# Kernel tuning notes

Hardware: AMD Instinct MI355X
Metric: run time of the kernel (lower is better)

The kernel has to match this reference:

```python
import jax, jax.numpy as jnp
import numpy as np

K = 3  # inferred kernel size (28->26->pool->13->11->pool->5 matches 32*5*5 FC input)


def _patches(x, k=K):
    # x: (N,C,H,W) -> (N,C,k*k,OH,OW) valid patches, stride 1
    N, C, H, W = x.shape
    OH, OW = H - k + 1, W - k + 1
    return jnp.stack(
        [x[:, :, i:i + OH, j:j + OW] for i in range(k) for j in range(k)], axis=2
    )


def _maxpool2(x):
    N, C, H, W = x.shape
    H2, W2 = H // 2, W // 2
    x = x[:, :, :H2 * 2, :W2 * 2].reshape(N, C, H2, 2, W2, 2)
    return x.max(axis=(3, 5))


def _lc2d(x, w, b):
    # unshared-weight locally connected conv: w (O,C,k*k,OH,OW), b (O,OH,OW)
    p = _patches(x)  # (N,C,k*k,OH,OW)
    return jnp.einsum('nckij,ockij->noij', p, w) + b


def setup_inputs():
    key = jax.random.key(0)
    ks = jax.random.split(key, 9)
    s = 0.05
    return {
        'x': jax.random.normal(ks[0], (4096, 1, 28, 28), jnp.float32),
        'w1': jax.random.normal(ks[1], (16, 1, 9, 26, 26), jnp.float32) * s,
        'b1': jax.random.normal(ks[2], (16, 26, 26), jnp.float32) * s,
        'w2': jax.random.normal(ks[3], (32, 16, 9, 11, 11), jnp.float32) * s,
        'b2': jax.random.normal(ks[4], (32, 11, 11), jnp.float32) * s,
        'fc1_w': jax.random.normal(ks[5], (32 * 5 * 5, 128), jnp.float32) * s,
        'fc1_b': jax.random.normal(ks[6], (128,), jnp.float32) * s,
        'fc2_w': jax.random.normal(ks[7], (128, 10), jnp.float32) * s,
        'fc2_b': jax.random.normal(ks[8], (10,), jnp.float32) * s,
    }


def reference(x, w1, b1, w2, b2, fc1_w, fc1_b, fc2_w, fc2_b):
    h = _maxpool2(jax.nn.relu(_lc2d(x, w1, b1)))      # (N,16,13,13)
    h = _maxpool2(jax.nn.relu(_lc2d(h, w2, b2)))      # (N,32,5,5)
    h = h.reshape(h.shape[0], -1)                      # (N,800)
    h = jax.nn.relu(h @ fc1_w + fc1_b)                 # (N,128)
    return h @ fc2_w + fc2_b                           # (N,10)
```

## Files before the change

kernel.cpp:

```cpp
#include <hip/hip_runtime.h>

#define NB 4096

typedef __attribute__((ext_vector_type(8))) short s8v;
typedef __attribute__((ext_vector_type(4))) float f4v;

#define H1B_OFF 6422528u
#define H2B_OFF 28573696u
#define W2B_OFF 35127296u
#define B2R_OFF 36765696u
#define W1B_OFF 36778496u
#define B1R_OFF 37470720u
#define WFB_OFF 37513984u

__device__ __forceinline__ unsigned short f2bf(float f) {
  unsigned int u = __builtin_bit_cast(unsigned int, f);
  u += 0x7fffu + ((u >> 16) & 1u);
  return (unsigned short)(u >> 16);
}

__global__ __launch_bounds__(256) void k_prep(const float* __restrict__ w1,
                                              const float* __restrict__ b1,
                                              const float* __restrict__ w2,
                                              const float* __restrict__ b2,
                                              const float* __restrict__ f1w,
                                              short* __restrict__ w1b,
                                              float* __restrict__ b1r,
                                              short* __restrict__ w2b,
                                              float* __restrict__ b2r,
                                              short* __restrict__ wfb) {
  const int bx = blockIdx.x;
  if (bx < 169) {
    const int q = bx * 256 + threadIdx.x;
    const int l = q & 63;
    const int cv = (q >> 6) & 3;
    const int pos = q >> 8;
    const int o = l & 15;
    const int i = pos / 13, j = pos % 13;
    const int dy = cv >> 1, dx = cv & 1;
    unsigned short v[8];
    #pragma unroll
    for (int t = 0; t < 8; t++) {
      const int k = (l >> 4) * 8 + t;
      float f = 0.f;
      if (k < 16) {
        const int py = k >> 2, px = k & 3;
        const int ky = py - dy, kx = px - dx;
        if (ky >= 0 && ky < 3 && kx >= 0 && kx < 3)
          f = w1[(o * 9 + ky * 3 + kx) * 676 + (2 * i + dy) * 26 + 2 * j + dx];
      }
      v[t] = f2bf(f);
    }
    *reinterpret_cast<s8v*>(&w1b[q * 8]) = *reinterpret_cast<const s8v*>(v);
  } else if (bx < 212) {
    const int idx = (bx - 169) * 256 + threadIdx.x;
    if (idx < 10816) {
      const int cv = idx & 3;
      const int o = (idx >> 2) & 15;
      const int pos = idx >> 6;
      const int i = pos / 13, j = pos % 13;
      b1r[idx] = b1[(o * 26 + 2 * i + (cv >> 1)) * 26 + 2 * j + (cv & 1)];
    }
  } else if (bx < 612) {
    const int q = (bx - 212) * 256 + threadIdx.x;
    const int l = q & 63;
    const int ot = (q >> 6) & 1;
    const int s = (q >> 7) & 7;
    const int cv = (q >> 10) & 3;
    const int pos = q >> 12;
    const int o = ot * 16 + (l & 15);
    const int dy = cv >> 1, dx = cv & 1;
    const int I = pos / 5, J = pos % 5;
    unsigned short v[8];
    #pragma unroll
    for (int t = 0; t < 8; t++) {
      const int k = s * 32 + (l >> 4) * 8 + t;
      const int w = k >> 4, c = k & 15;
      const int py = w >> 2, px = w & 3;
      const int ky = py - dy, kx = px - dx;
      float f = 0.f;
      if (ky >= 0 && ky < 3 && kx >= 0 && kx < 3)
        f = w2[((o * 16 + c) * 9 + ky * 3 + kx) * 121 +
               (2 * I + dy) * 11 + (2 * J + dx)];
      v[t] = f2bf(f);
    }
    *reinterpret_cast<s8v*>(&w2b[q * 8]) = *reinterpret_cast<const s8v*>(v);
  } else if (bx == 612) {
    for (int q = threadIdx.x; q < 3200; q += 256) {
      const int pos = q >> 7;
      const int r = q & 127;
      const int o = r >> 2, cv = r & 3;
      const int I = pos / 5, J = pos % 5;
      b2r[q] = b2[o * 121 + (2 * I + (cv >> 1)) * 11 + 2 * J + (cv & 1)];
    }
  } else {
    const int q = (bx - 613) * 256 + threadIdx.x;
    const int l = q & 63;
    const int jt = (q >> 6) & 7;
    const int s = q >> 9;
    const int j = jt * 16 + (l & 15);
    unsigned short v[8];
    #pragma unroll
    for (int t = 0; t < 8; t++) {
      const int o = (l >> 4) * 8 + t;
      v[t] = f2bf(f1w[(o * 25 + s) * 128 + j]);
    }
    *reinterpret_cast<s8v*>(&wfb[q * 8]) = *reinterpret_cast<const s8v*>(v);
  }
}

__global__ __launch_bounds__(256, 4) void k_lc1(const float* __restrict__ x,
                                                const short* __restrict__ w1b,
                                                const float* __restrict__ b1r,
                                                short* __restrict__ h1b) {
  __shared__ unsigned short ush[256 * 24];
  const int pos = blockIdx.y;
  const int i = pos / 13, j = pos % 13;
  const int tid = threadIdx.x;
  const int l = tid & 63;
  const int wv = tid >> 6;
  const int lm = l & 15, kg = l >> 4;
  const int n0b = blockIdx.x * 256;

  s8v bf[4];
  #pragma unroll
  for (int cv = 0; cv < 4; cv++)
    bf[cv] = *reinterpret_cast<const s8v*>(w1b + ((pos * 4 + cv) * 64 + l) * 8);
  const float4 bias = *reinterpret_cast<const float4*>(b1r + (pos * 16 + lm) * 4);

  f4v acc[4][4];
  #pragma unroll
  for (int a = 0; a < 4; a++)
    #pragma unroll
    for (int cv = 0; cv < 4; cv++) acc[a][cv] = (f4v){0.f, 0.f, 0.f, 0.f};

  const int col0 = (2 * i) * 28 + 2 * j;

  #pragma unroll
  for (int a = 0; a < 4; a++) {
    const int nl = n0b + wv * 64 + a * 16 + lm;
    s8v av = (s8v){0, 0, 0, 0, 0, 0, 0, 0};
    if (kg < 2) {
      const float* xr = x + nl * 784 + col0 + kg * 2 * 28;
      #pragma unroll
      for (int r = 0; r < 2; r++) {
        const float2 lo = *reinterpret_cast<const float2*>(xr + r * 28);
        const float2 hi = *reinterpret_cast<const float2*>(xr + r * 28 + 2);
        av[r * 4 + 0] = (short)f2bf(lo.x);
        av[r * 4 + 1] = (short)f2bf(lo.y);
        av[r * 4 + 2] = (short)f2bf(hi.x);
        av[r * 4 + 3] = (short)f2bf(hi.y);
      }
    }
    #pragma unroll
    for (int cv = 0; cv < 4; cv++)
      acc[a][cv] =
          __builtin_amdgcn_mfma_f32_16x16x32_bf16(av, bf[cv], acc[a][cv], 0, 0, 0);
  }

  #pragma unroll
  for (int a = 0; a < 4; a++) {
    #pragma unroll
    for (int reg = 0; reg < 4; reg++) {
      const int nl = wv * 64 + a * 16 + kg * 4 + reg;
      const float v =
          fmaxf(fmaxf(acc[a][0][reg] + bias.x, acc[a][1][reg] + bias.y),
                fmaxf(acc[a][2][reg] + bias.z, acc[a][3][reg] + bias.w));
      ush[nl * 24 + lm] = f2bf(fmaxf(v, 0.f));
    }
  }
  short* dst = h1b + (pos * 4096 + n0b + tid) * 16;
  const unsigned short* src = ush + tid * 24;
  *reinterpret_cast<s8v*>(dst) = *reinterpret_cast<const s8v*>(src);
  *reinterpret_cast<s8v*>(dst + 8) = *reinterpret_cast<const s8v*>(src + 8);
}

__global__ __launch_bounds__(256, 2) void k_lc2(const short* __restrict__ h1b,
                                                const short* __restrict__ w2b,
                                                const float* __restrict__ b2r,
                                                short* __restrict__ h2b) {
  __shared__ short sb[32768];
  const int pos = blockIdx.y;
  const int I = pos / 5, J = pos % 5;
  const int tid = threadIdx.x;
  const int l = tid & 63;
  const int wave = tid >> 6;
  const int wm = wave >> 1, ot = wave & 1;
  const int nw = blockIdx.x * 128 + wm * 64;
  const int kg = l >> 4;
  const int lm = l & 15;
  const int c0 = (kg & 1) * 8;
  const int whalf = kg >> 1;

  const short* wsrc = w2b + pos * 32768;
  #pragma unroll
  for (int r = 0; r < 16; r++) {
    const int idx = r * 256 + tid;
    *reinterpret_cast<s8v*>(&sb[idx * 8]) =
        *reinterpret_cast<const s8v*>(&wsrc[idx * 8]);
  }
  __syncthreads();

  f4v acc[4][4];
  #pragma unroll
  for (int a = 0; a < 4; a++)
    #pragma unroll
    for (int cv = 0; cv < 4; cv++)
      acc[a][cv] = (f4v){0.f, 0.f, 0.f, 0.f};

  #pragma unroll
  for (int s = 0; s < 8; s++) {
    const int wdw = s * 2 + whalf;
    const int py = wdw >> 2, px = wdw & 3;
    const int p = (2 * I + py) * 13 + (2 * J + px);
    const int abase = (p * 4096 + nw + lm) * 16 + c0;
    s8v av[4];
    #pragma unroll
    for (int a = 0; a < 4; a++)
      av[a] = *reinterpret_cast<const s8v*>(h1b + abase + a * 256);
    #pragma unroll
    for (int cv = 0; cv < 4; cv++) {
      const s8v bf = *reinterpret_cast<const s8v*>(
          &sb[(((cv * 8 + s) * 2 + ot) * 64 + l) * 8]);
      #pragma unroll
      for (int a = 0; a < 4; a++)
        acc[a][cv] =
            __builtin_amdgcn_mfma_f32_16x16x32_bf16(av[a], bf, acc[a][cv], 0, 0, 0);
    }
  }

  const int o = ot * 16 + lm;
  const float4 bias = *reinterpret_cast<const float4*>(b2r + (pos * 32 + o) * 4);
  #pragma unroll
  for (int a = 0; a < 4; a++) {
    const int nb = nw + a * 16 + kg * 4;
    #pragma unroll
    for (int reg = 0; reg < 4; reg++) {
      const float v =
          fmaxf(fmaxf(acc[a][0][reg] + bias.x, acc[a][1][reg] + bias.y),
                fmaxf(acc[a][2][reg] + bias.z, acc[a][3][reg] + bias.w));
      h2b[(pos * 4096 + nb + reg) * 32 + o] = (short)f2bf(fmaxf(v, 0.f));
    }
  }
}

__global__ __launch_bounds__(256) void k_fc(const short* __restrict__ h2b,
                                            const short* __restrict__ wfb,
                                            const float* __restrict__ f1b,
                                            const float* __restrict__ f2w,
                                            const float* __restrict__ f2b,
                                            float* __restrict__ out) {
  __shared__ float sh3[128 * 17];
  __shared__ float swf2[128 * 12];
  __shared__ float sb1[128];
  const int tid = threadIdx.x;
  const int l = tid & 63;
  const int w = tid >> 6;
  const int lm = l & 15, kg = l >> 4;
  const int n0 = blockIdx.x * 16;
  const int jt0 = w * 2;

  for (int idx = tid; idx < 1536; idx += 256) {
    const int kk = idx / 12, f = idx % 12;
    swf2[idx] = (f < 10) ? f2w[kk * 10 + f] : 0.f;
  }
  if (tid < 128) sb1[tid] = f1b[tid];

  f4v acc0 = (f4v){0.f, 0.f, 0.f, 0.f};
  f4v acc1 = (f4v){0.f, 0.f, 0.f, 0.f};

  #pragma unroll
  for (int s = 0; s < 25; s++) {
    const s8v av = *reinterpret_cast<const s8v*>(
        h2b + (s * 4096 + n0 + lm) * 32 + kg * 8);
    const s8v b0 = *reinterpret_cast<const s8v*>(
        wfb + ((s * 8 + jt0) * 64 + l) * 8);
    const s8v b1v = *reinterpret_cast<const s8v*>(
        wfb + ((s * 8 + jt0 + 1) * 64 + l) * 8);
    acc0 = __builtin_amdgcn_mfma_f32_16x16x32_bf16(av, b0, acc0, 0, 0, 0);
    acc1 = __builtin_amdgcn_mfma_f32_16x16x32_bf16(av, b1v, acc1, 0, 0, 0);
  }
  __syncthreads();

  #pragma unroll
  for (int q = 0; q < 2; q++) {
    const f4v a = q ? acc1 : acc0;
    const int j = (jt0 + q) * 16 + lm;
    #pragma unroll
    for (int reg = 0; reg < 4; reg++)
      sh3[j * 17 + kg * 4 + reg] = fmaxf(a[reg] + sb1[j], 0.f);
  }
  __syncthreads();

  if (tid < 160) {
    const int oo = tid >> 4, nn = tid & 15;
    float s = f2b[oo];
    for (int j = 0; j < 128; j++)
      s += sh3[j * 17 + nn] * swf2[j * 12 + oo];
    out[(n0 + nn) * 10 + oo] = s;
  }
}

extern "C" void kernel_launch(void* const* d_in, const int* in_sizes, int n_in,
                              void* d_out, int out_size, void* d_ws,
                              size_t ws_size, hipStream_t stream) {
  const float* x   = (const float*)d_in[0];
  const float* w1  = (const float*)d_in[1];
  const float* b1  = (const float*)d_in[2];
  const float* w2  = (const float*)d_in[3];
  const float* b2  = (const float*)d_in[4];
  const float* f1w = (const float*)d_in[5];
  const float* f1b = (const float*)d_in[6];
  const float* f2w = (const float*)d_in[7];
  const float* f2b = (const float*)d_in[8];
  float* out = (float*)d_out;
  char* ws = (char*)d_ws;
  short* h1b = (short*)(ws + H1B_OFF);
  short* h2b = (short*)(ws + H2B_OFF);
  short* w2b = (short*)(ws + W2B_OFF);
  float* b2r = (float*)(ws + B2R_OFF);
  short* w1b = (short*)(ws + W1B_OFF);
  float* b1r = (float*)(ws + B1R_OFF);
  short* wfb = (short*)(ws + WFB_OFF);

  k_prep<<<663, 256, 0, stream>>>(w1, b1, w2, b2, f1w,
                                  w1b, b1r, w2b, b2r, wfb);
  k_lc1<<<dim3(16, 169), 256, 0, stream>>>(x, w1b, b1r, h1b);
  k_lc2<<<dim3(32, 25), 256, 0, stream>>>(h1b, w2b, b2r, h2b);
  k_fc<<<256, 256, 0, stream>>>(h2b, wfb, f1b, f2w, f2b, out);
}
```

Before: 121.9 us.

## Stage lc1 input rows in LDS and loop over output columns per block

k_lc1 now launches one 64-thread block per output row and 64-sample tile. Each block loads the four needed input rows once from global memory, converts them to bf16 into LDS, then iterates over the 13 output columns reading patches from LDS. Weights and bias for the next column are prefetched in registers while the current one computes. This removes the repeated global reads and conversions of overlapping input patches, but cuts the grid to far fewer, smaller blocks and serialises 13 positions per wave, which may reduce latency hiding.

New measurement: 125.4 us. 1.03x slower.

```diff
diff --git a/kernel.cpp b/kernel.cpp
--- a/kernel.cpp
+++ b/kernel.cpp
@@ -4,6 +4,7 @@
 
 typedef __attribute__((ext_vector_type(8))) short s8v;
 typedef __attribute__((ext_vector_type(4))) float f4v;
+typedef __attribute__((ext_vector_type(4))) unsigned int ui4;
 
 #define H1B_OFF 6422528u
 #define H2B_OFF 28573696u
@@ -109,70 +110,107 @@
   }
 }
 
-__global__ __launch_bounds__(256, 4) void k_lc1(const float* __restrict__ x,
-                                                const short* __restrict__ w1b,
-                                                const float* __restrict__ b1r,
-                                                short* __restrict__ h1b) {
-  __shared__ unsigned short ush[256 * 24];
-  const int pos = blockIdx.y;
-  const int i = pos / 13, j = pos % 13;
-  const int tid = threadIdx.x;
-  const int l = tid & 63;
-  const int wv = tid >> 6;
+__global__ __launch_bounds__(64) void k_lc1(const float* __restrict__ x,
+                                            const short* __restrict__ w1b,
+                                            const float* __restrict__ b1r,
+                                            short* __restrict__ h1b) {
+  __shared__ unsigned short sx[64 * 122];
+  __shared__ unsigned short ush[64 * 24];
+  const int i = blockIdx.y;
+  const int l = threadIdx.x;
   const int lm = l & 15, kg = l >> 4;
-  const int n0b = blockIdx.x * 256;
-
-  s8v bf[4];
+  const int n0b = blockIdx.x * 64;
+
+  {
+    const int cq = l & 31;
+    const int half = l >> 5;
+    if (cq < 28) {
+      #pragma unroll 8
+      for (int q = 0; q < 32; q++) {
+        const int nr = q * 2 + half;
+        const float4 v = *reinterpret_cast<const float4*>(
+            x + (n0b + nr) * 784 + 56 * i + 4 * cq);
+        const unsigned int u0 =
+            ((unsigned int)f2bf(v.y) << 16) | f2bf(v.x);
+        const unsigned int u1 =
+            ((unsigned int)f2bf(v.w) << 16) | f2bf(v.z);
+        unsigned int* d =
+            reinterpret_cast<unsigned int*>(&sx[nr * 122 + 4 * cq]);
+        d[0] = u0;
+        d[1] = u1;
+      }
+    }
+  }
+
+  s8v bfA[4];
   #pragma unroll
   for (int cv = 0; cv < 4; cv++)
-    bf[cv] = *reinterpret_cast<const s8v*>(w1b + ((pos * 4 + cv) * 64 + l) * 8);
-  const float4 bias = *reinterpret_cast<const float4*>(b1r + (pos * 16 + lm) * 4);
-
-  f4v acc[4][4];
-  #pragma unroll
-  for (int a = 0; a < 4; a++)
-    #pragma unroll
-    for (int cv = 0; cv < 4; cv++) acc[a][cv] = (f4v){0.f, 0.f, 0.f, 0.f};
-
-  const int col0 = (2 * i) * 28 + 2 * j;
-
-  #pragma unroll
-  for (int a = 0; a < 4; a++) {
-    const int nl = n0b + wv * 64 + a * 16 + lm;
-    s8v av = (s8v){0, 0, 0, 0, 0, 0, 0, 0};
-    if (kg < 2) {
-      const float* xr = x + nl * 784 + col0 + kg * 2 * 28;
-      #pragma unroll
-      for (int r = 0; r < 2; r++) {
-        const float2 lo = *reinterpret_cast<const float2*>(xr + r * 28);
-        const float2 hi = *reinterpret_cast<const float2*>(xr + r * 28 + 2);
-        av[r * 4 + 0] = (short)f2bf(lo.x);
-        av[r * 4 + 1] = (short)f2bf(lo.y);
-        av[r * 4 + 2] = (short)f2bf(hi.x);
-        av[r * 4 + 3] = (short)f2bf(hi.y);
+    bfA[cv] = *reinterpret_cast<const s8v*>(
+        w1b + (((i * 13) * 4 + cv) * 64 + l) * 8);
+  float4 biasA = *reinterpret_cast<const float4*>(
+      b1r + ((i * 13) * 16 + lm) * 4);
+
+  for (int j = 0; j < 13; j++) {
+    const int pos = i * 13 + j;
+    s8v bfB[4];
+    float4 biasB;
+    const bool pf = (j < 12);
+    if (pf) {
+      #pragma unroll
+      for (int cv = 0; cv < 4; cv++)
+        bfB[cv] = *reinterpret_cast<const s8v*>(
+            w1b + (((pos + 1) * 4 + cv) * 64 + l) * 8);
+      biasB = *reinterpret_cast<const float4*>(
+          b1r + ((pos + 1) * 16 + lm) * 4);
+    }
+
+    f4v acc[4][4];
+    #pragma unroll
+    for (int a = 0; a < 4; a++)
+      #pragma unroll
+      for (int cv = 0; cv < 4; cv++) acc[a][cv] = (f4v){0.f, 0.f, 0.f, 0.f};
+
+    #pragma unroll
+    for (int a = 0; a < 4; a++) {
+      ui4 uav = (ui4){0u, 0u, 0u, 0u};
+      if (kg < 2) {
+        const int nl = a * 16 + lm;
+        const unsigned int* p0 = reinterpret_cast<const unsigned int*>(
+            &sx[nl * 122 + (2 * kg) * 28 + 2 * j]);
+        uav[0] = p0[0];
+        uav[1] = p0[1];
+        uav[2] = p0[14];
+        uav[3] = p0[15];
       }
-    }
-    #pragma unroll
-    for (int cv = 0; cv < 4; cv++)
-      acc[a][cv] =
-          __builtin_amdgcn_mfma_f32_16x16x32_bf16(av, bf[cv], acc[a][cv], 0, 0, 0);
-  }
-
-  #pragma unroll
-  for (int a = 0; a < 4; a++) {
-    #pragma unroll
-    for (int reg = 0; reg < 4; reg++) {
-      const int nl = wv * 64 + a * 16 + kg * 4 + reg;
-      const float v =
-          fmaxf(fmaxf(acc[a][0][reg] + bias.x, acc[a][1][reg] + bias.y),
-                fmaxf(acc[a][2][reg] + bias.z, acc[a][3][reg] + bias.w));
-      ush[nl * 24 + lm] = f2bf(fmaxf(v, 0.f));
-    }
-  }
-  short* dst = h1b + (pos * 4096 + n0b + tid) * 16;
-  const unsigned short* src = ush + tid * 24;
-  *reinterpret_cast<s8v*>(dst) = *reinterpret_cast<const s8v*>(src);
-  *reinterpret_cast<s8v*>(dst + 8) = *reinterpret_cast<const s8v*>(src + 8);
+      const s8v av = __builtin_bit_cast(s8v, uav);
+      #pragma unroll
+      for (int cv = 0; cv < 4; cv++)
+        acc[a][cv] = __builtin_amdgcn_mfma_f32_16x16x32_bf16(av, bfA[cv],
+                                                             acc[a][cv], 0, 0, 0);
+    }
+
+    #pragma unroll
+    for (int a = 0; a < 4; a++) {
+      #pragma unroll
+      for (int reg = 0; reg < 4; reg++) {
+        const int nl = a * 16 + kg * 4 + reg;
+        const float v =
+            fmaxf(fmaxf(acc[a][0][reg] + biasA.x, acc[a][1][reg] + biasA.y),
+                  fmaxf(acc[a][2][reg] + biasA.z, acc[a][3][reg] + biasA.w));
+        ush[nl * 24 + lm] = f2bf(fmaxf(v, 0.f));
+      }
+    }
+    short* dst = h1b + (pos * 4096 + n0b + l) * 16;
+    const unsigned short* src = ush + l * 24;
+    *reinterpret_cast<s8v*>(dst) = *reinterpret_cast<const s8v*>(src);
+    *reinterpret_cast<s8v*>(dst + 8) = *reinterpret_cast<const s8v*>(src + 8);
+
+    if (pf) {
+      #pragma unroll
+      for (int cv = 0; cv < 4; cv++) bfA[cv] = bfB[cv];
+      biasA = biasB;
+    }
+  }
 }
 
 __global__ __launch_bounds__(256, 2) void k_lc2(const short* __restrict__ h1b,
@@ -325,7 +363,7 @@
 
   k_prep<<<663, 256, 0, stream>>>(w1, b1, w2, b2, f1w,
                                   w1b, b1r, w2b, b2r, wfb);
-  k_lc1<<<dim3(16, 169), 256, 0, stream>>>(x, w1b, b1r, h1b);
+  k_lc1<<<dim3(64, 13), 64, 0, stream>>>(x, w1b, b1r, h1b);
   k_lc2<<<dim3(32, 25), 256, 0, stream>>>(h1b, w2b, b2r, h2b);
   k_fc<<<256, 256, 0, stream>>>(h2b, wfb, f1b, f2w, f2b, out);
 }
```
